# Performance work log

Measured on AMD Instinct MI355X. Metric: run time of the kernel, lower is better.

The kernel has to match this reference:

```python
import jax, jax.numpy as jnp
import numpy as np

LENGTH_SCALE = 0.1


def setup_inputs() -> dict:
    key = jax.random.key(0)
    k1, k2, k3 = jax.random.split(key, 3)
    features = jax.random.normal(k1, (8, 512, 128, 128), dtype=jnp.float32)
    # nn.Parameter init: normal(0, 0.05)
    weights = jax.random.normal(k2, (16, 64, 512), dtype=jnp.float32) * 0.05
    m = jax.random.normal(k3, (16, 64), dtype=jnp.float32)
    N = jnp.ones((64,), dtype=jnp.float32) * 12.0  # buffer init: ones * 12
    return {"features": features, "weights": weights, "m": m, "N": N}


def reference(features, weights, m, N):
    # per-class linear embedding projection: [b,f,h,w] x [e,c,f] -> [b,e,c,h,w]
    embeddings = jnp.einsum('bfhw,ecf->bechw', features, weights)
    centroids = m / N  # [e, c]
    gamma = -1.0 / (2.0 * LENGTH_SCALE ** 2)
    diff = embeddings - centroids[None, :, :, None, None]
    # squared L2, mean over embedding dim e, RBF exp -> [b, c, h, w]
    out = jnp.exp(jnp.mean(diff * diff, axis=1) * gamma)
    return out
```

## Files before the change

### kernel.cpp

```cpp
#include <hip/hip_runtime.h>

typedef __attribute__((ext_vector_type(8))) short bf16x8;
typedef __attribute__((ext_vector_type(4))) float f32x4;
typedef __attribute__((ext_vector_type(4))) float f4;
typedef __attribute__((ext_vector_type(2))) unsigned int u32x2;
typedef __attribute__((ext_vector_type(4))) unsigned int u32x4;

#define HW   16384
#define FDIM 512

__device__ __forceinline__ unsigned pkhi(float a, float b) {
    return __builtin_amdgcn_perm(__builtin_bit_cast(unsigned int, b),
                                 __builtin_bit_cast(unsigned int, a),
                                 0x07060302u);
}
__device__ __forceinline__ float trhi(float a) {
    return __builtin_bit_cast(float, __builtin_bit_cast(unsigned int, a) & 0xFFFF0000u);
}
__device__ __forceinline__ unsigned pklo(float a, float b) {
    return pkhi(a - trhi(a), b - trhi(b));
}

__global__ __launch_bounds__(256) void conv_w(const float* __restrict__ wts,
                                              unsigned short* __restrict__ wh,
                                              unsigned short* __restrict__ wl) {
    const int tid = blockIdx.x * 256 + threadIdx.x;
    const int n  = tid & 1023;
    const int kc = tid >> 10;
    const float* src = wts + (size_t)((n & 15) * 64 + (n >> 4)) * FDIM + kc * 8;
    f4 a = *(const f4*)src, b = *(const f4*)(src + 4);
    u32x4 h = { pkhi(a[0], a[1]), pkhi(a[2], a[3]), pkhi(b[0], b[1]), pkhi(b[2], b[3]) };
    u32x4 l = { pklo(a[0], a[1]), pklo(a[2], a[3]), pklo(b[0], b[1]), pklo(b[2], b[3]) };
    size_t off = ((size_t)kc * 1024 + n) * 8;
    *(u32x4*)(wh + off) = h;
    *(u32x4*)(wl + off) = l;
}

__global__ __launch_bounds__(256, 2) void duq_direct(
    const float* __restrict__ feat,
    const unsigned short* __restrict__ wh,
    const unsigned short* __restrict__ wl,
    const float* __restrict__ m_in,
    const float* __restrict__ n_in,
    float* __restrict__ out)
{
    const int t  = threadIdx.x;
    const int bx = blockIdx.x;
    const int kb = bx >> 3;
    const int nb = kb & 7;
    const int mb = (bx & 7) * 128 + (kb >> 3);
    const int bidx = mb >> 7;
    const int hw0  = (mb & 127) << 7;

    const int lane = t & 63;
    const int wv = t >> 6;
    const int wm = wv >> 1, wn = wv & 1;
    const int l16 = lane & 15, qd = lane >> 4;

    const float* apc = feat + (size_t)bidx * (FDIM * HW)
                     + (size_t)(qd * 8) * HW + (hw0 + wm * 64 + l16);

    const size_t bgoff = ((size_t)qd * 1024 + (size_t)(nb * 128 + wn * 64 + l16)) * 8;
    const unsigned short* bgh = wh + bgoff;
    const unsigned short* bgl = wl + bgoff;

    f32x4 acc[4][4] = {};

    bf16x8 cbh = *(const bf16x8*)(bgh);
    bf16x8 cbl = *(const bf16x8*)(bgl);
    size_t boff = 0;

    auto ldA = [&](float (&dst)[4][8]) {
        #pragma unroll
        for (int j = 0; j < 8; ++j) {
            const float* r = apc + (size_t)j * HW;
            #pragma unroll
            for (int i = 0; i < 4; ++i) dst[i][j] = r[i * 16];
        }
        apc += 32 * HW;
    };

    auto step = [&](float (&av)[4][8]) {
        bf16x8 fah[4], fal[4];
        #pragma unroll
        for (int i = 0; i < 4; ++i) {
            u32x4 hh = { pkhi(av[i][0], av[i][1]), pkhi(av[i][2], av[i][3]),
                         pkhi(av[i][4], av[i][5]), pkhi(av[i][6], av[i][7]) };
            u32x4 ll = { pklo(av[i][0], av[i][1]), pklo(av[i][2], av[i][3]),
                         pklo(av[i][4], av[i][5]), pklo(av[i][6], av[i][7]) };
            fah[i] = __builtin_bit_cast(bf16x8, hh);
            fal[i] = __builtin_bit_cast(bf16x8, ll);
        }
        #pragma unroll
        for (int j = 0; j < 4; ++j) {
            size_t bnext = boff + ((j == 3) ? (size_t)(32768 - 384) : (size_t)128);
            bf16x8 nbh = *(const bf16x8*)(bgh + bnext);
            bf16x8 nbl = *(const bf16x8*)(bgl + bnext);
            #pragma unroll
            for (int i = 0; i < 4; ++i) {
                acc[i][j] = __builtin_amdgcn_mfma_f32_16x16x32_bf16(fah[i], cbh, acc[i][j], 0, 0, 0);
                acc[i][j] = __builtin_amdgcn_mfma_f32_16x16x32_bf16(fah[i], cbl, acc[i][j], 0, 0, 0);
                acc[i][j] = __builtin_amdgcn_mfma_f32_16x16x32_bf16(fal[i], cbh, acc[i][j], 0, 0, 0);
            }
            cbh = nbh; cbl = nbl; boff = bnext;
        }
    };

    float avA[4][8], avB[4][8];
    ldA(avA);
    #pragma unroll 1
    for (int kt2 = 0; kt2 < 8; ++kt2) {
        ldA(avB);
        step(avA);
        if (kt2 < 7) ldA(avA);
        step(avB);
    }

    float centv[4];
    #pragma unroll
    for (int j = 0; j < 4; ++j) {
        int cj = nb * 8 + wn * 4 + j;
        centv[j] = m_in[l16 * 64 + cj] / n_in[cj];
    }
    #pragma unroll
    for (int i = 0; i < 4; ++i) {
        #pragma unroll
        for (int j = 0; j < 4; ++j) {
            float s0 = acc[i][j][0] - centv[j]; s0 *= s0;
            float s1 = acc[i][j][1] - centv[j]; s1 *= s1;
            float s2 = acc[i][j][2] - centv[j]; s2 *= s2;
            float s3 = acc[i][j][3] - centv[j]; s3 *= s3;
            #pragma unroll
            for (int msk = 1; msk < 16; msk <<= 1) {
                s0 += __shfl_xor(s0, msk, 64);
                s1 += __shfl_xor(s1, msk, 64);
                s2 += __shfl_xor(s2, msk, 64);
                s3 += __shfl_xor(s3, msk, 64);
            }
            if (l16 == 0) {
                int cj = nb * 8 + wn * 4 + j;
                f4 o;
                o[0] = __expf(s0 * -3.125f);
                o[1] = __expf(s1 * -3.125f);
                o[2] = __expf(s2 * -3.125f);
                o[3] = __expf(s3 * -3.125f);
                size_t off = ((size_t)(bidx * 64 + cj)) * HW
                           + (size_t)(hw0 + wm * 64 + i * 16 + qd * 4);
                *(f4*)(out + off) = o;
            }
        }
    }
}

__global__ __launch_bounds__(256) void duq_fallback(
    const float* __restrict__ feat, const float* __restrict__ wts,
    const float* __restrict__ m_in, const float* __restrict__ n_in,
    float* __restrict__ out)
{
    __shared__ __align__(16) unsigned short Ah[128 * 40];
    __shared__ __align__(16) unsigned short Al[128 * 40];
    __shared__ __align__(16) unsigned short Bh[128 * 40];
    __shared__ __align__(16) unsigned short Bl[128 * 40];

    const int t  = threadIdx.x;
    const int bx = blockIdx.x;
    const int nb = bx & 7;
    const int mb = bx >> 3;
    const int bidx = mb >> 7;
    const int hw0  = (mb & 127) << 7;

    const int fb = t & 7;
    const int pb = t >> 3;
    const float* ap = feat + (size_t)bidx * (FDIM * HW) + (size_t)(fb * 4) * HW + (hw0 + pb * 4);

    const int bn  = t >> 1;
    const int bh_ = t & 1;
    const int ng  = nb * 128 + bn;
    const float* bp = wts + (size_t)((ng & 15) * 64 + (ng >> 4)) * FDIM + bh_ * 16;

    unsigned short* awH = &Ah[(pb * 4) * 40 + fb * 4];
    unsigned short* awL = &Al[(pb * 4) * 40 + fb * 4];
    unsigned short* bwH = &Bh[bn * 40 + bh_ * 16];
    unsigned short* bwL = &Bl[bn * 40 + bh_ * 16];

    const int lane = t & 63;
    const int wv = t >> 6;
    const int wm = wv >> 1, wn = wv & 1;
    const int l16 = lane & 15, qd = lane >> 4;

    const unsigned short* arH = &Ah[(wm * 64 + l16) * 40 + qd * 8];
    const unsigned short* arL = &Al[(wm * 64 + l16) * 40 + qd * 8];
    const unsigned short* brH = &Bh[(wn * 64 + l16) * 40 + qd * 8];
    const unsigned short* brL = &Bl[(wn * 64 + l16) * 40 + qd * 8];

    f32x4 acc[4][4] = {};

    f4 av[4], bv[4];
    #pragma unroll
    for (int i = 0; i < 4; ++i) av[i] = *(const f4*)(ap + (size_t)i * HW);
    #pragma unroll
    for (int q = 0; q < 4; ++q) bv[q] = *(const f4*)(bp + q * 4);

    for (int kt = 0; kt < 16; ++kt) {
        __syncthreads();
        #pragma unroll
        for (int j = 0; j < 4; ++j) {
            float a0 = av[0][j], a1 = av[1][j], a2 = av[2][j], a3 = av[3][j];
            u32x2 h, l;
            h[0] = pkhi(a0, a1); h[1] = pkhi(a2, a3);
            l[0] = pklo(a0, a1); l[1] = pklo(a2, a3);
            *(u32x2*)(awH + j * 40) = h;
            *(u32x2*)(awL + j * 40) = l;
        }
        {
            u32x4 h0 = { pkhi(bv[0][0], bv[0][1]), pkhi(bv[0][2], bv[0][3]),
                         pkhi(bv[1][0], bv[1][1]), pkhi(bv[1][2], bv[1][3]) };
            u32x4 h1 = { pkhi(bv[2][0], bv[2][1]), pkhi(bv[2][2], bv[2][3]),
                         pkhi(bv[3][0], bv[3][1]), pkhi(bv[3][2], bv[3][3]) };
            u32x4 l0 = { pklo(bv[0][0], bv[0][1]), pklo(bv[0][2], bv[0][3]),
                         pklo(bv[1][0], bv[1][1]), pklo(bv[1][2], bv[1][3]) };
            u32x4 l1 = { pklo(bv[2][0], bv[2][1]), pklo(bv[2][2], bv[2][3]),
                         pklo(bv[3][0], bv[3][1]), pklo(bv[3][2], bv[3][3]) };
            *(u32x4*)(bwH)     = h0;  *(u32x4*)(bwH + 8) = h1;
            *(u32x4*)(bwL)     = l0;  *(u32x4*)(bwL + 8) = l1;
        }
        __syncthreads();

        if (kt < 15) {
            ap += 32 * HW;
            bp += 32;
            #pragma unroll
            for (int i = 0; i < 4; ++i) av[i] = *(const f4*)(ap + (size_t)i * HW);
            #pragma unroll
            for (int q = 0; q < 4; ++q) bv[q] = *(const f4*)(bp + q * 4);
        }

        bf16x8 fah[4], fal[4];
        #pragma unroll
        for (int i = 0; i < 4; ++i) {
            fah[i] = *(const bf16x8*)(arH + i * 640);
            fal[i] = *(const bf16x8*)(arL + i * 640);
        }
        #pragma unroll
        for (int j = 0; j < 4; ++j) {
            bf16x8 fbh = *(const bf16x8*)(brH + j * 640);
            bf16x8 fbl = *(const bf16x8*)(brL + j * 640);
            #pragma unroll
            for (int i = 0; i < 4; ++i) {
                acc[i][j] = __builtin_amdgcn_mfma_f32_16x16x32_bf16(fah[i], fbh, acc[i][j], 0, 0, 0);
                acc[i][j] = __builtin_amdgcn_mfma_f32_16x16x32_bf16(fah[i], fbl, acc[i][j], 0, 0, 0);
                acc[i][j] = __builtin_amdgcn_mfma_f32_16x16x32_bf16(fal[i], fbh, acc[i][j], 0, 0, 0);
            }
        }
    }

    float centv[4];
    #pragma unroll
    for (int j = 0; j < 4; ++j) {
        int cj = nb * 8 + wn * 4 + j;
        centv[j] = m_in[l16 * 64 + cj] / n_in[cj];
    }
    #pragma unroll
    for (int i = 0; i < 4; ++i) {
        #pragma unroll
        for (int j = 0; j < 4; ++j) {
            float s0 = acc[i][j][0] - centv[j]; s0 *= s0;
            float s1 = acc[i][j][1] - centv[j]; s1 *= s1;
            float s2 = acc[i][j][2] - centv[j]; s2 *= s2;
            float s3 = acc[i][j][3] - centv[j]; s3 *= s3;
            #pragma unroll
            for (int msk = 1; msk < 16; msk <<= 1) {
                s0 += __shfl_xor(s0, msk, 64);
                s1 += __shfl_xor(s1, msk, 64);
                s2 += __shfl_xor(s2, msk, 64);
                s3 += __shfl_xor(s3, msk, 64);
            }
            if (l16 == 0) {
                int cj = nb * 8 + wn * 4 + j;
                f4 o;
                o[0] = __expf(s0 * -3.125f);
                o[1] = __expf(s1 * -3.125f);
                o[2] = __expf(s2 * -3.125f);
                o[3] = __expf(s3 * -3.125f);
                size_t off = ((size_t)(bidx * 64 + cj)) * HW
                           + (size_t)(hw0 + wm * 64 + i * 16 + qd * 4);
                *(f4*)(out + off) = o;
            }
        }
    }
}

extern "C" void kernel_launch(void* const* d_in, const int* in_sizes, int n_in,
                              void* d_out, int out_size, void* d_ws, size_t ws_size,
                              hipStream_t stream) {
    const float* feat = (const float*)d_in[0];
    const float* wts  = (const float*)d_in[1];
    const float* mbuf = (const float*)d_in[2];
    const float* nbuf = (const float*)d_in[3];
    float* out = (float*)d_out;

    if (ws_size >= (size_t)(2 * 1024 * 1024 + 128 * 1024)) {
        unsigned short* wh = (unsigned short*)d_ws;
        unsigned short* wl = wh + 512 * 1024;
        conv_w<<<dim3(256), dim3(256), 0, stream>>>(wts, wh, wl);
        duq_direct<<<dim3(1024 * 8), dim3(256), 0, stream>>>(feat, wh, wl, mbuf, nbuf, out);
    } else {
        duq_fallback<<<dim3(1024 * 8), dim3(256), 0, stream>>>(feat, wts, mbuf, nbuf, out);
    }
}
```

Measured before the change: 691.7 us.

## Pre-split features into bf16 hi/lo blocked layout before MFMA kernel

Adds a pre-pass that converts the fp32 features into packed bf16 high/low pairs laid out k-chunk-major per pixel, so the main GEMM kernel can load MFMA operands directly from global memory without an in-kernel split or LDS staging. The main kernel double-buffers these A fragments while the three-MFMA hi/lo product runs. The cost is an extra pass that reads 256 MB and writes 256 MB of workspace, which the main kernel then reads back. This path only runs when the workspace is at least about 258 MB.

```diff
diff --git a/kernel.cpp b/kernel.cpp
--- a/kernel.cpp
+++ b/kernel.cpp
@@ -34,6 +34,132 @@
     size_t off = ((size_t)kc * 1024 + n) * 8;
     *(u32x4*)(wh + off) = h;
     *(u32x4*)(wl + off) = l;
+}
+
+__global__ __launch_bounds__(256) void conv_a(const float* __restrict__ feat,
+                                              unsigned short* __restrict__ ah,
+                                              unsigned short* __restrict__ al) {
+    const size_t tid = (size_t)blockIdx.x * 256 + threadIdx.x;
+    const int p    = (int)(tid & (HW - 1));
+    const int kc   = (int)((tid >> 14) & 63);
+    const int bidx = (int)(tid >> 20);
+    const float* src = feat + ((size_t)bidx * FDIM + (size_t)kc * 8) * HW + p;
+    float a[8];
+    #pragma unroll
+    for (int j = 0; j < 8; ++j) a[j] = src[(size_t)j * HW];
+    u32x4 h = { pkhi(a[0], a[1]), pkhi(a[2], a[3]), pkhi(a[4], a[5]), pkhi(a[6], a[7]) };
+    u32x4 l = { pklo(a[0], a[1]), pklo(a[2], a[3]), pklo(a[4], a[5]), pklo(a[6], a[7]) };
+    size_t off = tid * 8;
+    *(u32x4*)(ah + off) = h;
+    *(u32x4*)(al + off) = l;
+}
+
+__global__ __launch_bounds__(256, 2) void duq_pre(
+    const unsigned short* __restrict__ ah,
+    const unsigned short* __restrict__ al,
+    const unsigned short* __restrict__ wh,
+    const unsigned short* __restrict__ wl,
+    const float* __restrict__ m_in,
+    const float* __restrict__ n_in,
+    float* __restrict__ out)
+{
+    const int t  = threadIdx.x;
+    const int bx = blockIdx.x;
+    const int kb = bx >> 3;
+    const int nb = kb & 7;
+    const int mb = (bx & 7) * 128 + (kb >> 3);
+    const int bidx = mb >> 7;
+    const int hw0  = (mb & 127) << 7;
+
+    const int lane = t & 63;
+    const int wv = t >> 6;
+    const int wm = wv >> 1, wn = wv & 1;
+    const int l16 = lane & 15, qd = lane >> 4;
+
+    const size_t a0 = ((size_t)(bidx * 64 + qd) * HW + (size_t)(hw0 + wm * 64 + l16)) * 8;
+    const unsigned short* agh = ah + a0;
+    const unsigned short* agl = al + a0;
+
+    const size_t bgoff = ((size_t)qd * 1024 + (size_t)(nb * 128 + wn * 64 + l16)) * 8;
+    const unsigned short* bgh = wh + bgoff;
+    const unsigned short* bgl = wl + bgoff;
+
+    f32x4 acc[4][4] = {};
+
+    bf16x8 cbh = *(const bf16x8*)(bgh);
+    bf16x8 cbl = *(const bf16x8*)(bgl);
+    size_t boff = 0;
+
+    auto ldA = [&](bf16x8 (&dh)[4], bf16x8 (&dl)[4]) {
+        #pragma unroll
+        for (int i = 0; i < 4; ++i) {
+            dh[i] = *(const bf16x8*)(agh + i * 128);
+            dl[i] = *(const bf16x8*)(agl + i * 128);
+        }
+        agh += (size_t)4 * HW * 8;
+        agl += (size_t)4 * HW * 8;
+    };
+
+    auto step = [&](bf16x8 (&fah)[4], bf16x8 (&fal)[4]) {
+        #pragma unroll
+        for (int j = 0; j < 4; ++j) {
+            size_t bnext = boff + ((j == 3) ? (size_t)(32768 - 384) : (size_t)128);
+            bf16x8 nbh = *(const bf16x8*)(bgh + bnext);
+            bf16x8 nbl = *(const bf16x8*)(bgl + bnext);
+            #pragma unroll
+            for (int i = 0; i < 4; ++i) {
+                acc[i][j] = __builtin_amdgcn_mfma_f32_16x16x32_bf16(fah[i], cbh, acc[i][j], 0, 0, 0);
+                acc[i][j] = __builtin_amdgcn_mfma_f32_16x16x32_bf16(fah[i], cbl, acc[i][j], 0, 0, 0);
+                acc[i][j] = __builtin_amdgcn_mfma_f32_16x16x32_bf16(fal[i], cbh, acc[i][j], 0, 0, 0);
+            }
+            cbh = nbh; cbl = nbl; boff = bnext;
+        }
+    };
+
+    bf16x8 hA[4], lA[4], hB[4], lB[4];
+    ldA(hA, lA);
+    #pragma unroll 1
+    for (int kt2 = 0; kt2 < 8; ++kt2) {
+        ldA(hB, lB);
+        step(hA, lA);
+        if (kt2 < 7) ldA(hA, lA);
+        step(hB, lB);
+    }
+
+    float centv[4];
+    #pragma unroll
+    for (int j = 0; j < 4; ++j) {
+        int cj = nb * 8 + wn * 4 + j;
+        centv[j] = m_in[l16 * 64 + cj] / n_in[cj];
+    }
+    #pragma unroll
+    for (int i = 0; i < 4; ++i) {
+        #pragma unroll
+        for (int j = 0; j < 4; ++j) {
+            float s0 = acc[i][j][0] - centv[j]; s0 *= s0;
+            float s1 = acc[i][j][1] - centv[j]; s1 *= s1;
+            float s2 = acc[i][j][2] - centv[j]; s2 *= s2;
+            float s3 = acc[i][j][3] - centv[j]; s3 *= s3;
+            #pragma unroll
+            for (int msk = 1; msk < 16; msk <<= 1) {
+                s0 += __shfl_xor(s0, msk, 64);
+                s1 += __shfl_xor(s1, msk, 64);
+                s2 += __shfl_xor(s2, msk, 64);
+                s3 += __shfl_xor(s3, msk, 64);
+            }
+            if (l16 == 0) {
+                int cj = nb * 8 + wn * 4 + j;
+                f4 o;
+                o[0] = __expf(s0 * -3.125f);
+                o[1] = __expf(s1 * -3.125f);
+                o[2] = __expf(s2 * -3.125f);
+                o[3] = __expf(s3 * -3.125f);
+                size_t off = ((size_t)(bidx * 64 + cj)) * HW
+                           + (size_t)(hw0 + wm * 64 + i * 16 + qd * 4);
+                *(f4*)(out + off) = o;
+            }
+        }
+    }
 }
 
 __global__ __launch_bounds__(256, 2) void duq_direct(
@@ -299,11 +425,21 @@
     const float* nbuf = (const float*)d_in[3];
     float* out = (float*)d_out;
 
-    if (ws_size >= (size_t)(2 * 1024 * 1024 + 128 * 1024)) {
+    const size_t WS_MID = (size_t)(2 * 1024 * 1024 + 128 * 1024);
+    const size_t WS_BIG = WS_MID + (size_t)256 * 1024 * 1024;
+
+    if (ws_size >= WS_MID) {
         unsigned short* wh = (unsigned short*)d_ws;
         unsigned short* wl = wh + 512 * 1024;
         conv_w<<<dim3(256), dim3(256), 0, stream>>>(wts, wh, wl);
-        duq_direct<<<dim3(1024 * 8), dim3(256), 0, stream>>>(feat, wh, wl, mbuf, nbuf, out);
+        if (ws_size >= WS_BIG) {
+            unsigned short* ah = wh + WS_MID / 2;
+            unsigned short* al = ah + (size_t)64 * 1024 * 1024;
+            conv_a<<<dim3(32768), dim3(256), 0, stream>>>(feat, ah, al);
+            duq_pre<<<dim3(1024 * 8), dim3(256), 0, stream>>>(ah, al, wh, wl, mbuf, nbuf, out);
+        } else {
+            duq_direct<<<dim3(1024 * 8), dim3(256), 0, stream>>>(feat, wh, wl, mbuf, nbuf, out);
+        }
     } else {
         duq_fallback<<<dim3(1024 * 8), dim3(256), 0, stream>>>(feat, wts, mbuf, nbuf, out);
     }
```

Measured after the change: 760.5 us. 1.1x slower.

## Double per-block N tile to halve feature re-reads and block count

Applied to the files above, without the earlier changes.

Each block now computes 256 output columns (16 classes) instead of 128, so the grid shrinks from 8192 to 4096 blocks and each feature tile is loaded and split into bf16 hi/lo half as many times. The accumulator array doubles to 4x8 f32x4 per thread, and B fragments are prefetched through a 4-slot rotating register buffer three steps ahead. This cuts global feature traffic and conversion work, but raises register pressure, which may reduce occupancy or cause spills under the 2-blocks-per-SIMD launch bound.

```diff
diff --git a/kernel.cpp b/kernel.cpp
--- a/kernel.cpp
+++ b/kernel.cpp
@@ -36,7 +36,7 @@
     *(u32x4*)(wl + off) = l;
 }
 
-__global__ __launch_bounds__(256, 2) void duq_direct(
+__global__ __launch_bounds__(256, 2) void duq_fused(
     const float* __restrict__ feat,
     const unsigned short* __restrict__ wh,
     const unsigned short* __restrict__ wl,
@@ -46,9 +46,9 @@
 {
     const int t  = threadIdx.x;
     const int bx = blockIdx.x;
-    const int kb = bx >> 3;
-    const int nb = kb & 7;
-    const int mb = (bx & 7) * 128 + (kb >> 3);
+    const int kb  = bx >> 3;
+    const int nb2 = kb & 3;
+    const int mb  = (bx & 7) * 128 + (kb >> 2);
     const int bidx = mb >> 7;
     const int hw0  = (mb & 127) << 7;
 
@@ -60,22 +60,25 @@
     const float* apc = feat + (size_t)bidx * (FDIM * HW)
                      + (size_t)(qd * 8) * HW + (hw0 + wm * 64 + l16);
 
-    const size_t bgoff = ((size_t)qd * 1024 + (size_t)(nb * 128 + wn * 64 + l16)) * 8;
+    const size_t bgoff = ((size_t)qd * 1024 + (size_t)(nb2 * 256 + wn * 128 + l16)) * 8;
     const unsigned short* bgh = wh + bgoff;
     const unsigned short* bgl = wl + bgoff;
 
-    f32x4 acc[4][4] = {};
-
-    bf16x8 cbh = *(const bf16x8*)(bgh);
-    bf16x8 cbl = *(const bf16x8*)(bgl);
-    size_t boff = 0;
+    f32x4 acc[4][8] = {};
+
+    bf16x8 sh[4], sl[4];
+    sh[0] = *(const bf16x8*)(bgh);        sl[0] = *(const bf16x8*)(bgl);
+    sh[1] = *(const bf16x8*)(bgh + 128);  sl[1] = *(const bf16x8*)(bgl + 128);
+    sh[2] = *(const bf16x8*)(bgh + 256);  sl[2] = *(const bf16x8*)(bgl + 256);
+    const unsigned short* bkh = bgh;
+    const unsigned short* bkl = bgl;
 
     auto ldA = [&](float (&dst)[4][8]) {
         #pragma unroll
-        for (int j = 0; j < 8; ++j) {
-            const float* r = apc + (size_t)j * HW;
-            #pragma unroll
-            for (int i = 0; i < 4; ++i) dst[i][j] = r[i * 16];
+        for (int jk = 0; jk < 8; ++jk) {
+            const float* r = apc + (size_t)jk * HW;
+            #pragma unroll
+            for (int i = 0; i < 4; ++i) dst[i][jk] = r[i * 16];
         }
         apc += 32 * HW;
     };
@@ -92,18 +95,21 @@
             fal[i] = __builtin_bit_cast(bf16x8, ll);
         }
         #pragma unroll
-        for (int j = 0; j < 4; ++j) {
-            size_t bnext = boff + ((j == 3) ? (size_t)(32768 - 384) : (size_t)128);
-            bf16x8 nbh = *(const bf16x8*)(bgh + bnext);
-            bf16x8 nbl = *(const bf16x8*)(bgl + bnext);
+        for (int j = 0; j < 8; ++j) {
+            const int ls = (j + 3) & 3;
+            const size_t poff = (j < 5) ? (size_t)((j + 3) * 128)
+                                        : (size_t)(32768 + (j - 5) * 128);
+            sh[ls] = *(const bf16x8*)(bkh + poff);
+            sl[ls] = *(const bf16x8*)(bkl + poff);
+            const int us = j & 3;
             #pragma unroll
             for (int i = 0; i < 4; ++i) {
-                acc[i][j] = __builtin_amdgcn_mfma_f32_16x16x32_bf16(fah[i], cbh, acc[i][j], 0, 0, 0);
-                acc[i][j] = __builtin_amdgcn_mfma_f32_16x16x32_bf16(fah[i], cbl, acc[i][j], 0, 0, 0);
-                acc[i][j] = __builtin_amdgcn_mfma_f32_16x16x32_bf16(fal[i], cbh, acc[i][j], 0, 0, 0);
-            }
-            cbh = nbh; cbl = nbl; boff = bnext;
-        }
+                acc[i][j] = __builtin_amdgcn_mfma_f32_16x16x32_bf16(fah[i], sh[us], acc[i][j], 0, 0, 0);
+                acc[i][j] = __builtin_amdgcn_mfma_f32_16x16x32_bf16(fah[i], sl[us], acc[i][j], 0, 0, 0);
+                acc[i][j] = __builtin_amdgcn_mfma_f32_16x16x32_bf16(fal[i], sh[us], acc[i][j], 0, 0, 0);
+            }
+        }
+        bkh += 32768; bkl += 32768;
     };
 
     float avA[4][8], avB[4][8];
@@ -116,20 +122,16 @@
         step(avB);
     }
 
-    float centv[4];
-    #pragma unroll
-    for (int j = 0; j < 4; ++j) {
-        int cj = nb * 8 + wn * 4 + j;
-        centv[j] = m_in[l16 * 64 + cj] / n_in[cj];
-    }
     #pragma unroll
     for (int i = 0; i < 4; ++i) {
         #pragma unroll
-        for (int j = 0; j < 4; ++j) {
-            float s0 = acc[i][j][0] - centv[j]; s0 *= s0;
-            float s1 = acc[i][j][1] - centv[j]; s1 *= s1;
-            float s2 = acc[i][j][2] - centv[j]; s2 *= s2;
-            float s3 = acc[i][j][3] - centv[j]; s3 *= s3;
+        for (int j = 0; j < 8; ++j) {
+            const int cj = nb2 * 16 + wn * 8 + j;
+            const float cent = m_in[l16 * 64 + cj] / n_in[cj];
+            float s0 = acc[i][j][0] - cent; s0 *= s0;
+            float s1 = acc[i][j][1] - cent; s1 *= s1;
+            float s2 = acc[i][j][2] - cent; s2 *= s2;
+            float s3 = acc[i][j][3] - cent; s3 *= s3;
             #pragma unroll
             for (int msk = 1; msk < 16; msk <<= 1) {
                 s0 += __shfl_xor(s0, msk, 64);
@@ -138,7 +140,6 @@
                 s3 += __shfl_xor(s3, msk, 64);
             }
             if (l16 == 0) {
-                int cj = nb * 8 + wn * 4 + j;
                 f4 o;
                 o[0] = __expf(s0 * -3.125f);
                 o[1] = __expf(s1 * -3.125f);
@@ -303,7 +304,7 @@
         unsigned short* wh = (unsigned short*)d_ws;
         unsigned short* wl = wh + 512 * 1024;
         conv_w<<<dim3(256), dim3(256), 0, stream>>>(wts, wh, wl);
-        duq_direct<<<dim3(1024 * 8), dim3(256), 0, stream>>>(feat, wh, wl, mbuf, nbuf, out);
+        duq_fused<<<dim3(4096), dim3(256), 0, stream>>>(feat, wh, wl, mbuf, nbuf, out);
     } else {
         duq_fallback<<<dim3(1024 * 8), dim3(256), 0, stream>>>(feat, wts, mbuf, nbuf, out);
     }
```

Measured after the change: 676.0 us. 2.3% less time.
